# Kernel tuning notes

Measured on AMD Instinct MI355X. Metric: run time of the kernel, lower is better.

## Reference

```python
import jax, jax.numpy as jnp
import numpy as np
from jax import lax

D_MODEL = 1024
D_STATE = 16
D_CONV = 4
EXPAND = 2
INNER = EXPAND * D_MODEL


def setup_inputs() -> dict:
    key = jax.random.key(0)
    ks = jax.random.split(key, 8)
    B, L = 2, 1024
    x = jax.random.normal(ks[0], (B, L, D_MODEL), dtype=jnp.float32)
    W_in = jax.random.normal(ks[1], (2 * INNER, D_MODEL), dtype=jnp.float32) * (1.0 / np.sqrt(D_MODEL))
    conv_w = jax.random.normal(ks[2], (INNER, 1, D_CONV), dtype=jnp.float32) * (1.0 / np.sqrt(D_CONV))
    conv_b = jax.random.normal(ks[3], (INNER,), dtype=jnp.float32) * 0.02
    A = jax.random.normal(ks[4], (INNER, D_STATE), dtype=jnp.float32) * 0.1
    B_param = jax.random.normal(ks[5], (INNER, D_STATE), dtype=jnp.float32) * 0.1
    C_param = jax.random.normal(ks[6], (INNER, D_STATE), dtype=jnp.float32) * 0.1
    D_param = jnp.ones((INNER,), dtype=jnp.float32)
    W_out = jax.random.normal(ks[7], (D_MODEL, INNER), dtype=jnp.float32) * (1.0 / np.sqrt(INNER))
    return {"x": x, "W_in": W_in, "conv_w": conv_w, "conv_b": conv_b,
            "A": A, "B_param": B_param, "C_param": C_param, "D_param": D_param,
            "W_out": W_out}


def _mamba_fwd(x, W_in, conv_w, conv_b, A, B_param, C_param, W_out):
    Bsz, L, _ = x.shape
    inner = A.shape[0]
    # in_proj then interleaved split: view (B,L,inner,2) -> x=[...,0], gate=[...,1]
    xp = jnp.einsum('bld,ed->ble', x, W_in).reshape(Bsz, L, inner, 2)
    u, gate = xp[..., 0], xp[..., 1]
    # depthwise causal conv (torch pads both sides d_conv-1 then slices [:L] == left pad only)
    u_ncl = jnp.transpose(u, (0, 2, 1))  # (B, inner, L)
    conv = lax.conv_general_dilated(
        u_ncl, conv_w,
        window_strides=(1,), padding=[(D_CONV - 1, 0)],
        dimension_numbers=('NCH', 'OIH', 'NCH'),
        feature_group_count=inner)
    conv = conv + conv_b[None, :, None]
    xc = jnp.transpose(conv, (0, 2, 1))  # (B, L, inner)
    delta = jax.nn.sigmoid(xc)
    # discretized params, time-major for scan: (L, B, inner, d_state)
    a = jnp.transpose(A[None, None] * delta[..., None], (1, 0, 2, 3))
    bx = jnp.transpose(B_param[None, None] * (delta * xc)[..., None], (1, 0, 2, 3))

    def step(state, inp):
        a_l, bx_l = inp
        state = a_l * state + bx_l                       # (B, inner, d_state)
        y = jnp.einsum('bns,ns->bn', state, C_param)     # (B, inner)
        return state, y

    state0 = jnp.zeros((Bsz, inner, A.shape[1]), dtype=x.dtype)
    _, ys = lax.scan(step, state0, (a, bx))              # ys: (L, B, inner)
    out = jnp.transpose(ys, (1, 0, 2)) * jax.nn.sigmoid(gate)
    return jnp.einsum('bln,dn->bld', out, W_out)


def reference(x, W_in, conv_w, conv_b, A, B_param, C_param, D_param, W_out):
    # D_param is defined by the module but unused in its forward; kept for fidelity.
    return _mamba_fwd(x, W_in, conv_w, conv_b, A, B_param, C_param, W_out)
```

## Files before the change

### kernel.cpp

```cpp
#include <hip/hip_runtime.h>
#include <hip/hip_bf16.h>

#define D_MODEL 1024
#define INNER   2048
#define NPROJ   4096
#define BSZ     2
#define LSEQ    1024
#define MROWS   (BSZ*LSEQ)

#define CHUNK 32
#define WARM  24
#define NCHK  (LSEQ / CHUNK)

using short8   = __attribute__((ext_vector_type(8))) short;
using ushort8  = __attribute__((ext_vector_type(8))) unsigned short;
using f32x4    = __attribute__((ext_vector_type(4))) float;
typedef unsigned short ushort;

#define MFMA16(A,B,Cv) __builtin_amdgcn_mfma_f32_16x16x32_bf16(A,B,Cv,0,0,0)

__device__ __forceinline__ ushort tobf(float x) {
    return (ushort)(__builtin_bit_cast(unsigned, x) >> 16);
}
__device__ __forceinline__ float frombf(ushort h) {
    return __builtin_bit_cast(float, ((unsigned)h) << 16);
}
__device__ __forceinline__ void glds16(const void* g, void* l) {
    __builtin_amdgcn_global_load_lds((const __attribute__((address_space(1))) void*)g,
                                     (__attribute__((address_space(3))) void*)l, 16, 0, 0);
}

template<int K>
__device__ __forceinline__ void split_chunk(const float* __restrict__ in,
                                            ushort* __restrict__ hi,
                                            ushort* __restrict__ lo, int c) {
    int l = c & 63, sub = c >> 6;
    constexpr int KT = K / 32;
    int kt = sub % KT, rt = sub / KT;
    const float* src = in + (size_t)(rt * 16 + (l & 15)) * K + kt * 32 + (l >> 4) * 8;
    ushort8 h, lw;
#pragma unroll
    for (int j = 0; j < 8; ++j) {
        float x = src[j];
        h[j]  = tobf(x);
        lw[j] = tobf(x - frombf(h[j]));
    }
    *reinterpret_cast<ushort8*>(&hi[(size_t)c * 8]) = h;
    *reinterpret_cast<ushort8*>(&lo[(size_t)c * 8]) = lw;
}

template<int K>
__global__ __launch_bounds__(256) void splitbf_frag(const float* __restrict__ in,
                                                    ushort* __restrict__ hi,
                                                    ushort* __restrict__ lo, int nchunks) {
    int c = blockIdx.x * 256 + threadIdx.x;
    if (c >= nchunks) return;
    split_chunk<K>(in, hi, lo, c);
}

__global__ __launch_bounds__(256) void splitbf2_k(
    const float* __restrict__ in1, ushort* __restrict__ hi1, ushort* __restrict__ lo1, int n1,
    const float* __restrict__ in2, ushort* __restrict__ hi2, ushort* __restrict__ lo2, int n2) {
    int c = blockIdx.x * 256 + threadIdx.x;
    if (c < n1) {
        split_chunk<D_MODEL>(in1, hi1, lo1, c);
    } else {
        int cc = c - n1;
        if (cc < n2) split_chunk<D_MODEL>(in2, hi2, lo2, cc);
    }
}

template<int BN, int NCOL, int K, int SPLITK, bool PARTIAL, int NBUF, int NTHR>
__global__ __launch_bounds__(NTHR, 1) void gemm_pipe(
    const ushort* __restrict__ Agh, const ushort* __restrict__ Agl,
    const ushort* __restrict__ Bgh, const ushort* __restrict__ Bgl,
    float* __restrict__ C0, float* __restrict__ Crest)
{
    constexpr int BM = 128;
    constexpr int NW = NTHR / 64;
    constexpr int KT = K / 32;
    constexpr int NT = KT / SPLITK;
    constexpr int CB = (BN / 16) / NW;
    constexpr int CA = (BM / 16) / NW;
    __shared__ ushort Ah[NBUF][BM * 32], Al[NBUF][BM * 32];
    __shared__ ushort Bh[NBUF][BN * 32], Bl[NBUF][BN * 32];

    const int tid = threadIdx.x;
    const int wid = tid >> 6, lane = tid & 63;
    const int lm = lane & 15, lk = lane >> 4;

    constexpr int NTX = NCOL / BN;
    constexpr int NXY = NTX * (MROWS / BM);
    constexpr int CPX = NXY / 8;
    int lin = blockIdx.y * NTX + blockIdx.x;
    int swz = (lin & 7) * CPX + (lin >> 3);
    const int m0 = (swz / NTX) * BM, n0 = (swz % NTX) * BN;
    const int t0 = (SPLITK > 1 ? blockIdx.z : 0) * NT;
    const int wm = (NW == 8) ? (wid >> 2) * 64 : (wid >> 1) * 64;
    const int wn = (NW == 8) ? (wid & 3) * 64 : (wid & 1) * 64;

    f32x4 acc[4][4] = {};

    auto issueB = [&](const ushort* __restrict__ src, ushort* dst, int tg) {
#pragma unroll
        for (int ci = 0; ci < CB; ++ci) {
            int s = wid + ci * NW;
            const ushort* g = src + ((size_t)((n0 >> 4) + s) * KT + tg) * 512 + lane * 8;
            glds16(g, dst + s * 512);
        }
    };
    auto issueA = [&](const ushort* __restrict__ src, ushort* dst, int tg) {
#pragma unroll
        for (int ci = 0; ci < CA; ++ci) {
            int s = wid + ci * NW;
            const ushort* g = src + ((size_t)((m0 >> 4) + s) * KT + tg) * 512 + lane * 8;
            glds16(g, dst + s * 512);
        }
    };
    auto stageTile = [&](int t, int b) {
        issueB(Bgh, &Bh[b][0], t0 + t);
        issueB(Bgl, &Bl[b][0], t0 + t);
        issueA(Agh, &Ah[b][0], t0 + t);
        issueA(Agl, &Al[b][0], t0 + t);
    };

    if constexpr (NBUF == 3) {
        stageTile(0, 0);
        stageTile(1, 1);
        asm volatile("s_waitcnt vmcnt(6)" ::: "memory");
    } else {
        stageTile(0, 0);
        asm volatile("s_waitcnt vmcnt(0)" ::: "memory");
    }
    __builtin_amdgcn_s_barrier();

    short8 ah[4], bh[4];
#pragma unroll
    for (int i = 0; i < 4; ++i)
        ah[i] = *reinterpret_cast<const short8*>(&Ah[0][((wm >> 4) + i) * 512 + lane * 8]);
#pragma unroll
    for (int q = 0; q < 4; ++q)
        bh[q] = *reinterpret_cast<const short8*>(&Bh[0][((wn >> 4) + q) * 512 + lane * 8]);

    int cur = 0;
    for (int t = 0; t < NT; ++t) {
        int nxt, stg;
        bool pf;
        if constexpr (NBUF == 3) {
            nxt = cur + 1; if (nxt == 3) nxt = 0;
            stg = cur + 2; if (stg >= 3) stg -= 3;
            pf = (t + 2 < NT);
        } else {
            nxt = cur ^ 1;
            stg = nxt;
            pf = (t + 1 < NT);
        }
        const int tpre = (NBUF == 3) ? t + 2 : t + 1;
        short8 bl[4], al[4];

        asm volatile("s_waitcnt lgkmcnt(0)" ::: "memory");
        __builtin_amdgcn_sched_barrier(0);
        __builtin_amdgcn_s_setprio(1);
#pragma unroll
        for (int i = 0; i < 4; ++i)
#pragma unroll
            for (int q = 0; q < 4; ++q)
                acc[i][q] = MFMA16(ah[i], bh[q], acc[i][q]);
        __builtin_amdgcn_s_setprio(0);
#pragma unroll
        for (int q = 0; q < 4; ++q)
            bl[q] = *reinterpret_cast<const short8*>(&Bl[cur][((wn >> 4) + q) * 512 + lane * 8]);
        if (pf) issueB(Bgh, &Bh[stg][0], t0 + tpre);

        asm volatile("s_waitcnt lgkmcnt(0)" ::: "memory");
        __builtin_amdgcn_sched_barrier(0);
        __builtin_amdgcn_s_setprio(1);
#pragma unroll
        for (int i = 0; i < 4; ++i)
#pragma unroll
            for (int q = 0; q < 4; ++q)
                acc[i][q] = MFMA16(ah[i], bl[q], acc[i][q]);
        __builtin_amdgcn_s_setprio(0);
#pragma unroll
        for (int i = 0; i < 4; ++i)
            al[i] = *reinterpret_cast<const short8*>(&Al[cur][((wm >> 4) + i) * 512 + lane * 8]);
        if (pf) issueB(Bgl, &Bl[stg][0], t0 + tpre);
        __builtin_amdgcn_s_barrier();

        asm volatile("s_waitcnt lgkmcnt(0)" ::: "memory");
        __builtin_amdgcn_sched_barrier(0);
        __builtin_amdgcn_s_setprio(1);
#pragma unroll
        for (int i = 0; i < 4; ++i)
#pragma unroll
            for (int q = 0; q < 4; ++q)
                acc[i][q] = MFMA16(al[i], bh[q], acc[i][q]);
        __builtin_amdgcn_s_setprio(0);
        if (pf) {
            issueA(Agh, &Ah[stg][0], t0 + tpre);
            issueA(Agl, &Al[stg][0], t0 + tpre);
        }
        if (NBUF == 3 && pf) asm volatile("s_waitcnt vmcnt(6)" ::: "memory");
        else                 asm volatile("s_waitcnt vmcnt(0)" ::: "memory");
        __builtin_amdgcn_s_barrier();

        if (t + 1 < NT) {
#pragma unroll
            for (int i = 0; i < 4; ++i)
                ah[i] = *reinterpret_cast<const short8*>(&Ah[nxt][((wm >> 4) + i) * 512 + lane * 8]);
#pragma unroll
            for (int q = 0; q < 4; ++q)
                bh[q] = *reinterpret_cast<const short8*>(&Bh[nxt][((wn >> 4) + q) * 512 + lane * 8]);
        }
        cur = nxt;
    }

    float* C = C0;
    if constexpr (PARTIAL) {
        int kz = blockIdx.z;
        if (kz != 0) C = Crest + (size_t)(kz - 1) * MROWS * NCOL;
    }
#pragma unroll
    for (int i = 0; i < 4; ++i)
#pragma unroll
        for (int j = 0; j < 4; ++j)
#pragma unroll
            for (int r = 0; r < 4; ++r) {
                int row = m0 + wm + i * 16 + lk * 4 + r;
                int col = n0 + wn + j * 16 + lm;
                C[(size_t)row * NCOL + col] = acc[i][j][r];
            }
}

__global__ __launch_bounds__(256) void reduce_sk(float* __restrict__ out,
                                                 const float* __restrict__ rest) {
    constexpr size_t MN = (size_t)MROWS * D_MODEL;
    size_t i = ((size_t)blockIdx.x * 256 + threadIdx.x) * 4;
    f32x4 a = *reinterpret_cast<const f32x4*>(&out[i]);
    f32x4 b = *reinterpret_cast<const f32x4*>(&rest[i]);
    f32x4 c = *reinterpret_cast<const f32x4*>(&rest[MN + i]);
    f32x4 d = *reinterpret_cast<const f32x4*>(&rest[2 * MN + i]);
    *reinterpret_cast<f32x4*>(&out[i]) = (a + b) + (c + d);
}

__global__ __launch_bounds__(256) void scan_kernel(
    const float* __restrict__ xp,
    const float* __restrict__ conv_w, const float* __restrict__ conv_b,
    const float* __restrict__ Aa, const float* __restrict__ Bp, const float* __restrict__ Cp,
    ushort* __restrict__ yhi, ushort* __restrict__ ylo)
{
    const int NB = INNER / 256;
    int tid = threadIdx.x;
    int bi = blockIdx.x;
    int b  = bi / (NCHK * NB);
    int r  = bi % (NCHK * NB);
    int ch = r / NB;
    int n  = (r % NB) * 256 + tid;

    float4 w = *reinterpret_cast<const float4*>(&conv_w[n * 4]);
    float cb = conv_b[n];
    float An[16], Bn[16], Cn[16], st[16];
#pragma unroll
    for (int i = 0; i < 16; i += 4) {
        float4 va = *reinterpret_cast<const float4*>(&Aa[n * 16 + i]);
        float4 vb = *reinterpret_cast<const float4*>(&Bp[n * 16 + i]);
        float4 vc = *reinterpret_cast<const float4*>(&Cp[n * 16 + i]);
        An[i]=va.x; An[i+1]=va.y; An[i+2]=va.z; An[i+3]=va.w;
        Bn[i]=vb.x; Bn[i+1]=vb.y; Bn[i+2]=vb.z; Bn[i+3]=vb.w;
        Cn[i]=vc.x; Cn[i+1]=vc.y; Cn[i+2]=vc.z; Cn[i+3]=vc.w;
    }
#pragma unroll
    for (int s = 0; s < 16; ++s) st[s] = 0.f;

    int out0 = ch * CHUNK;
    int lstart = (out0 >= WARM) ? (out0 - WARM) : 0;
    float u0 = 0.f, u1 = 0.f, u2 = 0.f;
    const float* xb = xp + (size_t)b * LSEQ * NPROJ;
    size_t fcol = (size_t)(n >> 5) * 512 + ((n >> 3) & 3) * 128 + (n & 7);

    for (int l = lstart; l < out0; l += 8) {
        float uv[8];
#pragma unroll
        for (int i = 0; i < 8; ++i)
            uv[i] = xb[(size_t)(l + i) * NPROJ + 2 * n];
#pragma unroll
        for (int i = 0; i < 8; ++i) {
            float ul = uv[i];
            float xc = cb + w.x * u0 + w.y * u1 + w.z * u2 + w.w * ul;
            u0 = u1; u1 = u2; u2 = ul;
            float d = 1.f / (1.f + __expf(-xc));
            float dxc = d * xc;
#pragma unroll
            for (int s = 0; s < 16; ++s)
                st[s] = (An[s] * d) * st[s] + Bn[s] * dxc;
        }
    }
    for (int lt = 0; lt < CHUNK; lt += 8) {
        float uv[8], gv[8];
#pragma unroll
        for (int i = 0; i < 8; ++i) {
            float2 ug = *reinterpret_cast<const float2*>(
                &xb[(size_t)(out0 + lt + i) * NPROJ + 2 * n]);
            uv[i] = ug.x; gv[i] = ug.y;
        }
#pragma unroll
        for (int i = 0; i < 8; ++i) {
            float ul = uv[i];
            float xc = cb + w.x * u0 + w.y * u1 + w.z * u2 + w.w * ul;
            u0 = u1; u1 = u2; u2 = ul;
            float d = 1.f / (1.f + __expf(-xc));
            float dxc = d * xc;
            float y0 = 0.f, y1 = 0.f, y2 = 0.f, y3 = 0.f;
#pragma unroll
            for (int s = 0; s < 16; s += 4) {
                st[s + 0] = (An[s + 0] * d) * st[s + 0] + Bn[s + 0] * dxc;
                st[s + 1] = (An[s + 1] * d) * st[s + 1] + Bn[s + 1] * dxc;
                st[s + 2] = (An[s + 2] * d) * st[s + 2] + Bn[s + 2] * dxc;
                st[s + 3] = (An[s + 3] * d) * st[s + 3] + Bn[s + 3] * dxc;
                y0 += st[s + 0] * Cn[s + 0];
                y1 += st[s + 1] * Cn[s + 1];
                y2 += st[s + 2] * Cn[s + 2];
                y3 += st[s + 3] * Cn[s + 3];
            }
            float y = (y0 + y1) + (y2 + y3);
            float g = 1.f / (1.f + __expf(-gv[i]));
            float o = y * g;
            int R = b * LSEQ + out0 + lt + i;
            size_t fi = ((size_t)(R >> 4) * 64) * 512 + fcol + (R & 15) * 8;
            ushort hh = tobf(o);
            yhi[fi] = hh;
            ylo[fi] = tobf(o - frombf(hh));
        }
    }
}

extern "C" void kernel_launch(void* const* d_in, const int* in_sizes, int n_in,
                              void* d_out, int out_size, void* d_ws, size_t ws_size,
                              hipStream_t stream) {
    const float* x      = (const float*)d_in[0];
    const float* W_in   = (const float*)d_in[1];
    const float* conv_w = (const float*)d_in[2];
    const float* conv_b = (const float*)d_in[3];
    const float* A      = (const float*)d_in[4];
    const float* Bp     = (const float*)d_in[5];
    const float* Cp     = (const float*)d_in[6];
    const float* W_out  = (const float*)d_in[8];
    float* out = (float*)d_out;

    char* ws = (char*)d_ws;
    float* xp    = (float*)ws;
    ushort* Whi  = (ushort*)(ws + (32u << 20));
    ushort* Wlo  = (ushort*)(ws + (40u << 20));
    ushort* yghi = Whi;
    ushort* yglo = Wlo;
    ushort* Wohi = (ushort*)ws;
    ushort* Wolo = (ushort*)(ws + (4u << 20));
    float*  Prest = (float*)(ws + (8u << 20));
    ushort* xhi = (ushort*)d_out;
    ushort* xlo = xhi + (size_t)MROWS * D_MODEL;

    dim3 blk(256);
    const int n1 = NPROJ * D_MODEL / 8;
    const int n2 = MROWS * D_MODEL / 8;
    splitbf2_k<<<dim3((n1 + n2) / 256), blk, 0, stream>>>(
        W_in, Whi, Wlo, n1, x, xhi, xlo, n2);
    gemm_pipe<256, NPROJ, D_MODEL, 1, false, 3, 512>
        <<<dim3(16, 16), dim3(512), 0, stream>>>(xhi, xlo, Whi, Wlo, xp, nullptr);
    scan_kernel<<<dim3(BSZ * NCHK * (INNER / 256)), blk, 0, stream>>>(
        xp, conv_w, conv_b, A, Bp, Cp, yghi, yglo);
    splitbf_frag<INNER><<<dim3((D_MODEL * INNER / 8) / 256), blk, 0, stream>>>(
        W_out, Wohi, Wolo, D_MODEL * INNER / 8);
    gemm_pipe<128, D_MODEL, INNER, 4, true, 2, 256>
        <<<dim3(8, 16, 4), dim3(256), 0, stream>>>(yghi, yglo, Wohi, Wolo, out, Prest);
    reduce_sk<<<dim3((MROWS * D_MODEL / 4) / 256), blk, 0, stream>>>(out, Prest);
}
```

Before: 124.0 us.

## Replace bf16 split in-projection GEMM with two-level int8 quantized MFMA GEMM

Quantizes W_in and x per row into int8 high and low residual bytes with a per-row scale, stored directly in MFMA fragment layout. A new int8 GEMM uses 16x16x64 i8 MFMAs with a three-buffer LDS pipeline and rescales the accumulators in the epilogue. The goal is to halve operand bytes and double MFMA throughput relative to the bf16 hi/lo scheme. The risk is lower accuracy from per-row int8 quantization, since the low byte gives roughly 15 bits of effective mantissa.

```diff
diff --git a/kernel.cpp b/kernel.cpp
--- a/kernel.cpp
+++ b/kernel.cpp
@@ -15,9 +15,13 @@
 using short8   = __attribute__((ext_vector_type(8))) short;
 using ushort8  = __attribute__((ext_vector_type(8))) unsigned short;
 using f32x4    = __attribute__((ext_vector_type(4))) float;
+using i32x4    = __attribute__((ext_vector_type(4))) int;
+using char16v  = __attribute__((ext_vector_type(16))) char;
 typedef unsigned short ushort;
+typedef unsigned char uchar;
 
 #define MFMA16(A,B,Cv) __builtin_amdgcn_mfma_f32_16x16x32_bf16(A,B,Cv,0,0,0)
+#define MFMAI8(A,B,Cv) __builtin_amdgcn_mfma_i32_16x16x64_i8(A,B,Cv,0,0,0)
 
 __device__ __forceinline__ ushort tobf(float x) {
     return (ushort)(__builtin_bit_cast(unsigned, x) >> 16);
@@ -28,6 +32,190 @@
 __device__ __forceinline__ void glds16(const void* g, void* l) {
     __builtin_amdgcn_global_load_lds((const __attribute__((address_space(1))) void*)g,
                                      (__attribute__((address_space(3))) void*)l, 16, 0, 0);
+}
+
+__global__ __launch_bounds__(256) void quant_rows(
+    const float* __restrict__ W, uchar* __restrict__ Wh, uchar* __restrict__ Wl,
+    float* __restrict__ sW, int RW,
+    const float* __restrict__ X, uchar* __restrict__ Xh, uchar* __restrict__ Xl,
+    float* __restrict__ sX)
+{
+    const int K = 1024, KT64 = K / 64;
+    int gw = blockIdx.x * 4 + (threadIdx.x >> 6);
+    int lane = threadIdx.x & 63;
+    const float* src; uchar *dh, *dl; float* ss; int r;
+    if (gw < RW) { r = gw;      src = W + (size_t)r * K; dh = Wh; dl = Wl; ss = sW; }
+    else         { r = gw - RW; src = X + (size_t)r * K; dh = Xh; dl = Xl; ss = sX; }
+
+    float v[16];
+#pragma unroll
+    for (int p = 0; p < 4; ++p) {
+        float4 f = *reinterpret_cast<const float4*>(src + lane * 16 + p * 4);
+        v[p*4+0] = f.x; v[p*4+1] = f.y; v[p*4+2] = f.z; v[p*4+3] = f.w;
+    }
+    float mx = 0.f;
+#pragma unroll
+    for (int j = 0; j < 16; ++j) mx = fmaxf(mx, fabsf(v[j]));
+#pragma unroll
+    for (int off = 1; off < 64; off <<= 1) mx = fmaxf(mx, __shfl_xor(mx, off));
+    float s1 = fmaxf(mx, 1e-20f) / 127.f;
+    if (lane == 0) ss[r] = s1;
+    float inv = 1.f / s1;
+    char16v hb, lb;
+#pragma unroll
+    for (int j = 0; j < 16; ++j) {
+        float t = v[j] * inv;
+        float h = rintf(t);
+        float l = rintf((t - h) * 256.f);
+        l = fminf(fmaxf(l, -128.f), 127.f);
+        hb[j] = (char)(int)h;
+        lb[j] = (char)(int)l;
+    }
+    size_t byte = (((size_t)(r >> 4) * KT64 + (lane >> 2)) * 64
+                   + ((lane & 3) << 4) + (r & 15)) * 16;
+    *reinterpret_cast<i32x4*>(dh + byte) = *reinterpret_cast<const i32x4*>(&hb);
+    *reinterpret_cast<i32x4*>(dl + byte) = *reinterpret_cast<const i32x4*>(&lb);
+}
+
+__global__ __launch_bounds__(512, 1) void gemm1_i8(
+    const uchar* __restrict__ Xh, const uchar* __restrict__ Xl, const float* __restrict__ sX,
+    const uchar* __restrict__ Wh, const uchar* __restrict__ Wl, const float* __restrict__ sW,
+    float* __restrict__ C)
+{
+    constexpr int KT64 = D_MODEL / 64;
+    constexpr int NT = 16;
+    __shared__ uchar Ah[3][8192], Al[3][8192];
+    __shared__ uchar Bh[3][16384], Bl[3][16384];
+
+    const int tid = threadIdx.x;
+    const int wid = tid >> 6, lane = tid & 63;
+    const int lm = lane & 15, lk = lane >> 4;
+
+    constexpr int NTX = NPROJ / 256;
+    constexpr int CPX = (NTX * (MROWS / 128)) / 8;
+    int lin = blockIdx.y * NTX + blockIdx.x;
+    int swz = (lin & 7) * CPX + (lin >> 3);
+    const int m0 = (swz / NTX) * 128, n0 = (swz % NTX) * 256;
+    const int wm = (wid >> 2) * 64, wn = (wid & 3) * 64;
+
+    i32x4 acc1[4][4] = {};
+    i32x4 acc2[4][4] = {};
+
+    auto issueB = [&](const uchar* __restrict__ src, uchar* dst, int t, int ci) {
+        int s = wid + ci * 8;
+        const uchar* g = src + ((size_t)((n0 >> 4) + s) * KT64 + t) * 1024 + lane * 16;
+        glds16(g, dst + s * 1024);
+    };
+    auto issueA = [&](const uchar* __restrict__ src, uchar* dst, int t) {
+        const uchar* g = src + ((size_t)((m0 >> 4) + wid) * KT64 + t) * 1024 + lane * 16;
+        glds16(g, dst + wid * 1024);
+    };
+    auto stageTile = [&](int t, int b) {
+        issueB(Wh, &Bh[b][0], t, 0); issueB(Wh, &Bh[b][0], t, 1);
+        issueB(Wl, &Bl[b][0], t, 0); issueB(Wl, &Bl[b][0], t, 1);
+        issueA(Xh, &Ah[b][0], t);    issueA(Xl, &Al[b][0], t);
+    };
+
+    stageTile(0, 0);
+    stageTile(1, 1);
+    asm volatile("s_waitcnt vmcnt(6)" ::: "memory");
+    __builtin_amdgcn_s_barrier();
+
+    i32x4 ah[4], bh[4];
+#pragma unroll
+    for (int i = 0; i < 4; ++i)
+        ah[i] = *reinterpret_cast<const i32x4*>(&Ah[0][((wm >> 4) + i) * 1024 + lane * 16]);
+#pragma unroll
+    for (int q = 0; q < 4; ++q)
+        bh[q] = *reinterpret_cast<const i32x4*>(&Bh[0][((wn >> 4) + q) * 1024 + lane * 16]);
+
+    int cur = 0;
+    for (int t = 0; t < NT; ++t) {
+        int nxt = cur + 1; if (nxt == 3) nxt = 0;
+        int stg = cur + 2; if (stg >= 3) stg -= 3;
+        const bool pf = (t + 2 < NT);
+        i32x4 bl[4], al[4];
+
+        asm volatile("s_waitcnt lgkmcnt(0)" ::: "memory");
+        __builtin_amdgcn_sched_barrier(0);
+        __builtin_amdgcn_s_setprio(1);
+#pragma unroll
+        for (int i = 0; i < 4; ++i)
+#pragma unroll
+            for (int q = 0; q < 4; ++q)
+                acc1[i][q] = MFMAI8(ah[i], bh[q], acc1[i][q]);
+        __builtin_amdgcn_s_setprio(0);
+#pragma unroll
+        for (int q = 0; q < 4; ++q)
+            bl[q] = *reinterpret_cast<const i32x4*>(&Bl[cur][((wn >> 4) + q) * 1024 + lane * 16]);
+        if (pf) {
+            issueB(Wh, &Bh[stg][0], t + 2, 0);
+            issueB(Wh, &Bh[stg][0], t + 2, 1);
+        }
+
+        asm volatile("s_waitcnt lgkmcnt(0)" ::: "memory");
+        __builtin_amdgcn_sched_barrier(0);
+        __builtin_amdgcn_s_setprio(1);
+#pragma unroll
+        for (int i = 0; i < 4; ++i)
+#pragma unroll
+            for (int q = 0; q < 4; ++q)
+                acc2[i][q] = MFMAI8(ah[i], bl[q], acc2[i][q]);
+        __builtin_amdgcn_s_setprio(0);
+#pragma unroll
+        for (int i = 0; i < 4; ++i)
+            al[i] = *reinterpret_cast<const i32x4*>(&Al[cur][((wm >> 4) + i) * 1024 + lane * 16]);
+        if (pf) {
+            issueB(Wl, &Bl[stg][0], t + 2, 0);
+            issueB(Wl, &Bl[stg][0], t + 2, 1);
+        }
+        __builtin_amdgcn_s_barrier();
+
+        asm volatile("s_waitcnt lgkmcnt(0)" ::: "memory");
+        __builtin_amdgcn_sched_barrier(0);
+        __builtin_amdgcn_s_setprio(1);
+#pragma unroll
+        for (int i = 0; i < 4; ++i)
+#pragma unroll
+            for (int q = 0; q < 4; ++q)
+                acc2[i][q] = MFMAI8(al[i], bh[q], acc2[i][q]);
+        __builtin_amdgcn_s_setprio(0);
+        if (pf) {
+            issueA(Xh, &Ah[stg][0], t + 2);
+            issueA(Xl, &Al[stg][0], t + 2);
+        }
+        if (pf) asm volatile("s_waitcnt vmcnt(6)" ::: "memory");
+        else    asm volatile("s_waitcnt vmcnt(0)" ::: "memory");
+        __builtin_amdgcn_s_barrier();
+
+        if (t + 1 < NT) {
+#pragma unroll
+            for (int i = 0; i < 4; ++i)
+                ah[i] = *reinterpret_cast<const i32x4*>(&Ah[nxt][((wm >> 4) + i) * 1024 + lane * 16]);
+#pragma unroll
+            for (int q = 0; q < 4; ++q)
+                bh[q] = *reinterpret_cast<const i32x4*>(&Bh[nxt][((wn >> 4) + q) * 1024 + lane * 16]);
+        }
+        cur = nxt;
+    }
+
+#pragma unroll
+    for (int i = 0; i < 4; ++i) {
+        int r0 = m0 + wm + i * 16 + lk * 4;
+        float4 s4 = *reinterpret_cast<const float4*>(&sX[r0]);
+        float sa[4] = {s4.x, s4.y, s4.z, s4.w};
+#pragma unroll
+        for (int j = 0; j < 4; ++j) {
+            int col = n0 + wn + j * 16 + lm;
+            float sb = sW[col];
+#pragma unroll
+            for (int r = 0; r < 4; ++r) {
+                float o = sa[r] * sb *
+                    ((float)acc1[i][j][r] + (float)acc2[i][j][r] * 0.00390625f);
+                C[(size_t)(r0 + r) * NPROJ + col] = o;
+            }
+        }
+    }
 }
 
 template<int K>
@@ -56,18 +244,6 @@
     int c = blockIdx.x * 256 + threadIdx.x;
     if (c >= nchunks) return;
     split_chunk<K>(in, hi, lo, c);
-}
-
-__global__ __launch_bounds__(256) void splitbf2_k(
-    const float* __restrict__ in1, ushort* __restrict__ hi1, ushort* __restrict__ lo1, int n1,
-    const float* __restrict__ in2, ushort* __restrict__ hi2, ushort* __restrict__ lo2, int n2) {
-    int c = blockIdx.x * 256 + threadIdx.x;
-    if (c < n1) {
-        split_chunk<D_MODEL>(in1, hi1, lo1, c);
-    } else {
-        int cc = c - n1;
-        if (cc < n2) split_chunk<D_MODEL>(in2, hi2, lo2, cc);
-    }
 }
 
 template<int BN, int NCOL, int K, int SPLITK, bool PARTIAL, int NBUF, int NTHR>
@@ -349,23 +525,23 @@
 
     char* ws = (char*)d_ws;
     float* xp    = (float*)ws;
-    ushort* Whi  = (ushort*)(ws + (32u << 20));
-    ushort* Wlo  = (ushort*)(ws + (40u << 20));
-    ushort* yghi = Whi;
-    ushort* yglo = Wlo;
+    uchar* Wh8   = (uchar*)(ws + (32u << 20));
+    uchar* Wl8   = (uchar*)(ws + (36u << 20));
+    float* sW    = (float*)(ws + (40u << 20));
+    ushort* yghi = (ushort*)(ws + (32u << 20));
+    ushort* yglo = (ushort*)(ws + (40u << 20));
     ushort* Wohi = (ushort*)ws;
     ushort* Wolo = (ushort*)(ws + (4u << 20));
     float*  Prest = (float*)(ws + (8u << 20));
-    ushort* xhi = (ushort*)d_out;
-    ushort* xlo = xhi + (size_t)MROWS * D_MODEL;
+    uchar* xh8 = (uchar*)d_out;
+    uchar* xl8 = xh8 + (2u << 20);
+    float* sX  = (float*)(xh8 + (4u << 20));
 
     dim3 blk(256);
-    const int n1 = NPROJ * D_MODEL / 8;
-    const int n2 = MROWS * D_MODEL / 8;
-    splitbf2_k<<<dim3((n1 + n2) / 256), blk, 0, stream>>>(
-        W_in, Whi, Wlo, n1, x, xhi, xlo, n2);
-    gemm_pipe<256, NPROJ, D_MODEL, 1, false, 3, 512>
-        <<<dim3(16, 16), dim3(512), 0, stream>>>(xhi, xlo, Whi, Wlo, xp, nullptr);
+    quant_rows<<<dim3((NPROJ + MROWS) / 4), blk, 0, stream>>>(
+        W_in, Wh8, Wl8, sW, NPROJ, x, xh8, xl8, sX);
+    gemm1_i8<<<dim3(16, 16), dim3(512), 0, stream>>>(
+        xh8, xl8, sX, Wh8, Wl8, sW, xp);
     scan_kernel<<<dim3(BSZ * NCHK * (INNER / 256)), blk, 0, stream>>>(
         xp, conv_w, conv_b, A, Bp, Cp, yghi, yglo);
     splitbf_frag<INNER><<<dim3((D_MODEL * INNER / 8) / 256), blk, 0, stream>>>(
```

New measurement: 104.7 us. 1.18x faster.
